# Kernel optimization log

Hardware: AMD Instinct MI355X
Metric: run time of the kernel (lower is better)

Reference implementation:

```python
import jax, jax.numpy as jnp
import numpy as np

N_NODES = 100000
N_EDGES = 3200000
IN_DIM = 128


def setup_inputs() -> dict:
    key = jax.random.key(0)
    ks = jax.random.split(key, 6)
    x = jax.random.normal(ks[0], (N_NODES, IN_DIM), dtype=jnp.float32)
    edge_index = jax.random.randint(ks[1], (2, N_EDGES), 0, N_NODES, dtype=jnp.int64)
    # Glorot-ish init for weights, zero bias (PyG GCNConv default has bias)
    W1 = jax.random.normal(ks[2], (IN_DIM, 32), dtype=jnp.float32) / np.sqrt(IN_DIM)
    b1 = jnp.zeros((32,), dtype=jnp.float32)
    W2 = jax.random.normal(ks[3], (32, 16), dtype=jnp.float32) / np.sqrt(32.0)
    b2 = jnp.zeros((16,), dtype=jnp.float32)
    Wf = jax.random.normal(ks[4], (16, 1), dtype=jnp.float32) / np.sqrt(16.0)
    bf = jnp.zeros((1,), dtype=jnp.float32)
    return {"x": x, "edge_index": edge_index, "W1": W1, "b1": b1,
            "W2": W2, "b2": b2, "Wf": Wf, "bf": bf}


def reference(x, edge_index, W1, b1, W2, b2, Wf, bf):
    N = x.shape[0]
    # PyG GCNConv: add self-loops, symmetric normalization D^-1/2 (A+I) D^-1/2
    loop = jnp.arange(N, dtype=edge_index.dtype)
    src = jnp.concatenate([edge_index[0], loop])  # message sources (x_j)
    dst = jnp.concatenate([edge_index[1], loop])  # aggregation targets
    deg = jax.ops.segment_sum(jnp.ones_like(dst, dtype=x.dtype), dst, num_segments=N)
    dinv = jax.lax.rsqrt(jnp.maximum(deg, 1.0))  # deg >= 1 due to self-loops
    norm = dinv[src] * dinv[dst]                  # per-edge coefficient

    def gcn_conv(h, W, b):
        h = h @ W                                 # linear transform first (small dim)
        msg = h[src] * norm[:, None]              # gather + scale
        return jax.ops.segment_sum(msg, dst, num_segments=N) + b  # scatter-add

    h = jax.nn.relu(gcn_conv(x, W1, b1))
    h = jax.nn.relu(gcn_conv(h, W2, b2))
    return (h @ Wf + bf).squeeze(-1)              # [N]
```

## Files before the change

kernel.cpp:

```cpp
#include <hip/hip_runtime.h>


#define TPB 256
#define NBUCK 256
#define BCAP 16384
#define CHUNK 8192

__device__ __forceinline__ unsigned f2bf(float f) {
    unsigned u = __float_as_uint(f);
    return (u + 0x7FFFu + ((u >> 16) & 1u)) >> 16;
}
__device__ __forceinline__ float bflo(unsigned u) { return __uint_as_float(u << 16); }
__device__ __forceinline__ float bfhi(unsigned u) { return __uint_as_float(u & 0xFFFF0000u); }

__global__ void zero_bcursor_kernel(int* __restrict__ bcur) {
    bcur[threadIdx.x] = 0;
}

__global__ __launch_bounds__(256) void binA2_kernel(
        const int* __restrict__ src, const int* __restrict__ dst,
        int* __restrict__ bcur, unsigned* __restrict__ staging, int E, int NPB) {
    __shared__ unsigned packed[CHUNK];
    __shared__ unsigned char buckb[CHUNK];
    __shared__ int hist[NBUCK];
    __shared__ int scan_[NBUCK];
    __shared__ int lstart[NBUCK];
    __shared__ int lcur[NBUCK];
    __shared__ int gbase[NBUCK];
    int tid = threadIdx.x;
    int start = blockIdx.x * CHUNK;
    int sz = min(CHUNK, E - start);

    hist[tid] = 0;
    __syncthreads();
    for (int i = tid; i < sz; i += 256) {
        unsigned d = (unsigned)dst[start + i];
        atomicAdd(&hist[d / (unsigned)NPB], 1);
    }
    __syncthreads();
    int v = hist[tid];
    scan_[tid] = v;
    __syncthreads();
    for (int dd = 1; dd < NBUCK; dd <<= 1) {
        int t = 0;
        if (tid >= dd) t = scan_[tid - dd];
        __syncthreads();
        scan_[tid] += t;
        __syncthreads();
    }
    lstart[tid] = scan_[tid] - v;
    lcur[tid] = 0;
    gbase[tid] = atomicAdd(&bcur[tid], v);
    __syncthreads();
    for (int i = tid; i < sz; i += 256) {
        unsigned d = (unsigned)dst[start + i];
        unsigned s = (unsigned)src[start + i];
        unsigned b = d / (unsigned)NPB;
        unsigned loc = d - b * (unsigned)NPB;
        int pos = atomicAdd(&lcur[b], 1);
        int si = lstart[b] + pos;
        packed[si] = (loc << 20) | s;
        buckb[si] = (unsigned char)b;
    }
    __syncthreads();
    for (int i = tid; i < sz; i += 256) {
        unsigned b = buckb[i];
        int dsti = gbase[b] + (i - lstart[b]);
        if (dsti < BCAP)
            staging[(size_t)b * BCAP + dsti] = packed[i];
    }
}

__global__ void bucket_scan_kernel(const int* __restrict__ bcur, int* __restrict__ bbase) {
    __shared__ int s[NBUCK];
    int tid = threadIdx.x;
    int v = min(bcur[tid], BCAP);
    s[tid] = v;
    __syncthreads();
    for (int d = 1; d < NBUCK; d <<= 1) {
        int t = 0;
        if (tid >= d) t = s[tid - d];
        __syncthreads();
        s[tid] += t;
        __syncthreads();
    }
    bbase[tid] = s[tid] - v;
}

__global__ void buildB_kernel(const int* __restrict__ bcur, const int* __restrict__ bbase,
                              const unsigned* __restrict__ staging,
                              int* __restrict__ offs, int* __restrict__ counts,
                              float* __restrict__ dinv, int* __restrict__ csr_src,
                              int N, int NPB) {
    __shared__ int hist[512];
    __shared__ int scan_[512];
    __shared__ int cur[512];
    int b = blockIdx.x;
    int tid = threadIdx.x;
    int sz = min(bcur[b], BCAP);
    int base = bbase[b];
    int n0 = b * NPB;
    int nn = min(NPB, N - n0);
    const unsigned* se = staging + (size_t)b * BCAP;

    hist[tid] = 0;
    __syncthreads();
    for (int i = tid; i < sz; i += 512)
        atomicAdd(&hist[se[i] >> 20], 1);
    __syncthreads();
    int h = hist[tid];
    scan_[tid] = h;
    __syncthreads();
    for (int d = 1; d < 512; d <<= 1) {
        int t = 0;
        if (tid >= d) t = scan_[tid - d];
        __syncthreads();
        scan_[tid] += t;
        __syncthreads();
    }
    int excl = scan_[tid] - h;
    cur[tid] = excl;
    if (tid < nn) {
        int node = n0 + tid;
        offs[node] = base + excl;
        counts[node] = h;
        dinv[node] = rsqrtf((float)(h + 1));
    }
    __syncthreads();
    for (int i = tid; i < sz; i += 512) {
        unsigned p = se[i];
        int pos = atomicAdd(&cur[p >> 20], 1);
        csr_src[base + pos] = (int)(p & 0xFFFFFu);
    }
}

__global__ __launch_bounds__(256) void gemm1_kernel(
        const float* __restrict__ x, const float* __restrict__ W1,
        const float* __restrict__ dinv, unsigned* __restrict__ xwd, int N) {
    __shared__ float ws_[128 * 32];
    for (int i = threadIdx.x; i < 128 * 32; i += blockDim.x) ws_[i] = W1[i];
    __syncthreads();
    int t = threadIdx.x;
    int node = blockIdx.x * 64 + (t >> 2);
    if (node >= N) return;
    int jq = (t & 3) * 8;
    float acc[8];
#pragma unroll
    for (int j = 0; j < 8; ++j) acc[j] = 0.0f;
    const float4* xr = (const float4*)(x + (size_t)node * 128);
#pragma unroll 4
    for (int k4 = 0; k4 < 32; ++k4) {
        float4 xv = xr[k4];
        const float* wb = ws_ + (k4 * 4) * 32 + jq;
        float4 a0 = *(const float4*)(wb);
        float4 a1 = *(const float4*)(wb + 4);
        float4 b0 = *(const float4*)(wb + 32);
        float4 b1v = *(const float4*)(wb + 36);
        float4 c0 = *(const float4*)(wb + 64);
        float4 c1 = *(const float4*)(wb + 68);
        float4 d0 = *(const float4*)(wb + 96);
        float4 d1 = *(const float4*)(wb + 100);
        acc[0] += xv.x * a0.x + xv.y * b0.x + xv.z * c0.x + xv.w * d0.x;
        acc[1] += xv.x * a0.y + xv.y * b0.y + xv.z * c0.y + xv.w * d0.y;
        acc[2] += xv.x * a0.z + xv.y * b0.z + xv.z * c0.z + xv.w * d0.z;
        acc[3] += xv.x * a0.w + xv.y * b0.w + xv.z * c0.w + xv.w * d0.w;
        acc[4] += xv.x * a1.x + xv.y * b1v.x + xv.z * c1.x + xv.w * d1.x;
        acc[5] += xv.x * a1.y + xv.y * b1v.y + xv.z * c1.y + xv.w * d1.y;
        acc[6] += xv.x * a1.z + xv.y * b1v.z + xv.z * c1.z + xv.w * d1.z;
        acc[7] += xv.x * a1.w + xv.y * b1v.w + xv.z * c1.w + xv.w * d1.w;
    }
    float d = dinv[node];
    unsigned pk0 = f2bf(acc[0] * d) | (f2bf(acc[1] * d) << 16);
    unsigned pk1 = f2bf(acc[2] * d) | (f2bf(acc[3] * d) << 16);
    unsigned pk2 = f2bf(acc[4] * d) | (f2bf(acc[5] * d) << 16);
    unsigned pk3 = f2bf(acc[6] * d) | (f2bf(acc[7] * d) << 16);
    ((uint4*)(xwd + (size_t)node * 16))[t & 3] = make_uint4(pk0, pk1, pk2, pk3);
}

__global__ void agg32h_kernel(const int* __restrict__ offs, const int* __restrict__ counts,
                              const int* __restrict__ csr_src, const float* __restrict__ dinv,
                              const unsigned* __restrict__ xwd, float* __restrict__ agg, int N) {
    int wave = threadIdx.x >> 6;
    int lane = threadIdx.x & 63;
    int node = blockIdx.x * 4 + wave;
    if (node >= N) return;
    int q = lane & 3;
    int g = lane >> 2;
    int off = offs[node];
    int deg = counts[node];
    float acc[8];
#pragma unroll
    for (int k = 0; k < 8; ++k) acc[k] = 0.f;
    if (g == 0) {
        uint4 v = ((const uint4*)(xwd + (size_t)node * 16))[q];
        acc[0] = bflo(v.x); acc[1] = bfhi(v.x);
        acc[2] = bflo(v.y); acc[3] = bfhi(v.y);
        acc[4] = bflo(v.z); acc[5] = bfhi(v.z);
        acc[6] = bflo(v.w); acc[7] = bfhi(v.w);
    }
    int i = g;
    for (; i + 16 < deg; i += 32) {
        int s0 = csr_src[off + i];
        int s1 = csr_src[off + i + 16];
        uint4 v0 = ((const uint4*)(xwd + (size_t)s0 * 16))[q];
        uint4 v1 = ((const uint4*)(xwd + (size_t)s1 * 16))[q];
        acc[0] += bflo(v0.x) + bflo(v1.x); acc[1] += bfhi(v0.x) + bfhi(v1.x);
        acc[2] += bflo(v0.y) + bflo(v1.y); acc[3] += bfhi(v0.y) + bfhi(v1.y);
        acc[4] += bflo(v0.z) + bflo(v1.z); acc[5] += bfhi(v0.z) + bfhi(v1.z);
        acc[6] += bflo(v0.w) + bflo(v1.w); acc[7] += bfhi(v0.w) + bfhi(v1.w);
    }
    for (; i < deg; i += 16) {
        int s = csr_src[off + i];
        uint4 v = ((const uint4*)(xwd + (size_t)s * 16))[q];
        acc[0] += bflo(v.x); acc[1] += bfhi(v.x);
        acc[2] += bflo(v.y); acc[3] += bfhi(v.y);
        acc[4] += bflo(v.z); acc[5] += bfhi(v.z);
        acc[6] += bflo(v.w); acc[7] += bfhi(v.w);
    }
#pragma unroll
    for (int d = 32; d >= 4; d >>= 1) {
#pragma unroll
        for (int k = 0; k < 8; ++k) acc[k] += __shfl_down(acc[k], d, 64);
    }
    if (g == 0) {
        float dv = dinv[node];
        float* op = agg + (size_t)node * 32 + q * 8;
        ((float4*)op)[0] = make_float4(acc[0] * dv, acc[1] * dv, acc[2] * dv, acc[3] * dv);
        ((float4*)op)[1] = make_float4(acc[4] * dv, acc[5] * dv, acc[6] * dv, acc[7] * dv);
    }
}

__global__ void gemm2_kernel(const float* __restrict__ agg1, const float* __restrict__ W2,
                             const float* __restrict__ b1, const float* __restrict__ dinv,
                             unsigned* __restrict__ h2wd, int N) {
    __shared__ float ws_[32 * 16];
    __shared__ float bs_[32];
    for (int i = threadIdx.x; i < 32 * 16; i += blockDim.x) ws_[i] = W2[i];
    if (threadIdx.x < 32) bs_[threadIdx.x] = b1[threadIdx.x];
    __syncthreads();
    int node = blockIdx.x * blockDim.x + threadIdx.x;
    if (node >= N) return;
    float h[32];
    const float4* ar = (const float4*)(agg1 + (size_t)node * 32);
#pragma unroll
    for (int k4 = 0; k4 < 8; ++k4) {
        float4 v = ar[k4];
        h[k4 * 4 + 0] = fmaxf(v.x + bs_[k4 * 4 + 0], 0.0f);
        h[k4 * 4 + 1] = fmaxf(v.y + bs_[k4 * 4 + 1], 0.0f);
        h[k4 * 4 + 2] = fmaxf(v.z + bs_[k4 * 4 + 2], 0.0f);
        h[k4 * 4 + 3] = fmaxf(v.w + bs_[k4 * 4 + 3], 0.0f);
    }
    float acc[16];
#pragma unroll
    for (int j = 0; j < 16; ++j) acc[j] = 0.0f;
#pragma unroll
    for (int k = 0; k < 32; ++k) {
        float hv = h[k];
#pragma unroll
        for (int j4 = 0; j4 < 4; ++j4) {
            float4 w = *(const float4*)(ws_ + k * 16 + j4 * 4);
            acc[j4 * 4 + 0] += hv * w.x;
            acc[j4 * 4 + 1] += hv * w.y;
            acc[j4 * 4 + 2] += hv * w.z;
            acc[j4 * 4 + 3] += hv * w.w;
        }
    }
    float d = dinv[node];
    unsigned pk[8];
#pragma unroll
    for (int j = 0; j < 8; ++j)
        pk[j] = f2bf(acc[2 * j] * d) | (f2bf(acc[2 * j + 1] * d) << 16);
    uint4* hp = (uint4*)(h2wd + (size_t)node * 8);
    hp[0] = make_uint4(pk[0], pk[1], pk[2], pk[3]);
    hp[1] = make_uint4(pk[4], pk[5], pk[6], pk[7]);
}

__global__ void agg16h_kernel(const int* __restrict__ offs, const int* __restrict__ counts,
                              const int* __restrict__ csr_src, const float* __restrict__ dinv,
                              const unsigned* __restrict__ h2wd, float* __restrict__ agg, int N) {
    int wave = threadIdx.x >> 6;
    int lane = threadIdx.x & 63;
    int node = blockIdx.x * 4 + wave;
    if (node >= N) return;
    int q = lane & 1;
    int g = lane >> 1;
    int off = offs[node];
    int deg = counts[node];
    float acc[8];
#pragma unroll
    for (int k = 0; k < 8; ++k) acc[k] = 0.f;
    if (g == 0) {
        uint4 v = ((const uint4*)(h2wd + (size_t)node * 8))[q];
        acc[0] = bflo(v.x); acc[1] = bfhi(v.x);
        acc[2] = bflo(v.y); acc[3] = bfhi(v.y);
        acc[4] = bflo(v.z); acc[5] = bfhi(v.z);
        acc[6] = bflo(v.w); acc[7] = bfhi(v.w);
    }
    for (int i = g; i < deg; i += 32) {
        int s = csr_src[off + i];
        uint4 v = ((const uint4*)(h2wd + (size_t)s * 8))[q];
        acc[0] += bflo(v.x); acc[1] += bfhi(v.x);
        acc[2] += bflo(v.y); acc[3] += bfhi(v.y);
        acc[4] += bflo(v.z); acc[5] += bfhi(v.z);
        acc[6] += bflo(v.w); acc[7] += bfhi(v.w);
    }
#pragma unroll
    for (int d = 32; d >= 2; d >>= 1) {
#pragma unroll
        for (int k = 0; k < 8; ++k) acc[k] += __shfl_down(acc[k], d, 64);
    }
    if (g == 0) {
        float dv = dinv[node];
        float* op = agg + (size_t)node * 16 + q * 8;
        ((float4*)op)[0] = make_float4(acc[0] * dv, acc[1] * dv, acc[2] * dv, acc[3] * dv);
        ((float4*)op)[1] = make_float4(acc[4] * dv, acc[5] * dv, acc[6] * dv, acc[7] * dv);
    }
}

__global__ void final_kernel(const float* __restrict__ agg2, const float* __restrict__ b2,
                             const float* __restrict__ Wf, const float* __restrict__ bf,
                             float* __restrict__ out, int N) {
    int i = blockIdx.x * blockDim.x + threadIdx.x;
    if (i >= N) return;
    const float4* ar = (const float4*)(agg2 + (size_t)i * 16);
    float acc = bf[0];
#pragma unroll
    for (int j4 = 0; j4 < 4; ++j4) {
        float4 v = ar[j4];
        acc += fmaxf(v.x + b2[j4 * 4 + 0], 0.0f) * Wf[j4 * 4 + 0];
        acc += fmaxf(v.y + b2[j4 * 4 + 1], 0.0f) * Wf[j4 * 4 + 1];
        acc += fmaxf(v.z + b2[j4 * 4 + 2], 0.0f) * Wf[j4 * 4 + 2];
        acc += fmaxf(v.w + b2[j4 * 4 + 3], 0.0f) * Wf[j4 * 4 + 3];
    }
    out[i] = acc;
}

extern "C" void kernel_launch(void* const* d_in, const int* in_sizes, int n_in,
                              void* d_out, int out_size, void* d_ws, size_t ws_size,
                              hipStream_t stream) {
    const float* x  = (const float*)d_in[0];
    const int*   ei = (const int*)d_in[1];
    const float* W1 = (const float*)d_in[2];
    const float* b1 = (const float*)d_in[3];
    const float* W2 = (const float*)d_in[4];
    const float* b2 = (const float*)d_in[5];
    const float* Wf = (const float*)d_in[6];
    const float* bf = (const float*)d_in[7];

    int N = in_sizes[0] / 128;
    int E = in_sizes[1] / 2;
    const int* src = ei;
    const int* dst = ei + E;
    int NPB = (N + NBUCK - 1) / NBUCK;

    size_t Np = ((size_t)N + 3) & ~(size_t)3;
    size_t Ep = ((size_t)E + 3) & ~(size_t)3;
    int* wsI      = (int*)d_ws;
    int* counts   = wsI;
    int* offs     = counts + Np;
    int* bcur     = offs + Np;
    int* bbase    = bcur + NBUCK;
    int* csr_src  = bbase + NBUCK;
    float* dinv   = (float*)(csr_src + Ep);
    unsigned* xwd = (unsigned*)(dinv + Np);
    float* agg1   = (float*)(xwd + 16 * Np);
    unsigned* h2wd= (unsigned*)(agg1 + 32 * Np);
    float* agg2   = (float*)(h2wd + 8 * Np);
    float* out    = (float*)d_out;
    unsigned* staging = (unsigned*)agg1;

    int nbG1 = (N + 63) / 64;
    int nbC = (E + CHUNK - 1) / CHUNK;
    int nbN = (N + TPB - 1) / TPB;
    int nbW = (N + 3) / 4;

    zero_bcursor_kernel<<<1, NBUCK, 0, stream>>>(bcur);
    binA2_kernel<<<nbC, 256, 0, stream>>>(src, dst, bcur, staging, E, NPB);
    bucket_scan_kernel<<<1, NBUCK, 0, stream>>>(bcur, bbase);
    buildB_kernel<<<NBUCK, 512, 0, stream>>>(bcur, bbase, staging, offs, counts,
                                             dinv, csr_src, N, NPB);
    gemm1_kernel<<<nbG1, 256, 0, stream>>>(x, W1, dinv, xwd, N);
    agg32h_kernel<<<nbW, TPB, 0, stream>>>(offs, counts, csr_src, dinv, xwd, agg1, N);
    gemm2_kernel<<<nbN, TPB, 0, stream>>>(agg1, W2, b1, dinv, h2wd, N);
    agg16h_kernel<<<nbW, TPB, 0, stream>>>(offs, counts, csr_src, dinv, h2wd, agg2, N);
    final_kernel<<<nbN, TPB, 0, stream>>>(agg2, b2, Wf, bf, out, N);
}
```

Before: 286.5 us.

## Remap aggregation to few lanes per node and fuse final layer

Both aggregation kernels now give each node 4 lanes (layer 1) or 2 lanes (layer 2) instead of a full 64-lane wave. Each lane walks the whole neighbor list serially with 2-way unrolling, so the cross-lane shuffle reductions go away. With an average degree near 33, the old mapping left many lanes idle; the new one raises occupancy per node but serializes the neighbor walk and makes the CSR index reads less coalesced. The final linear+ReLU layer is fused into the second aggregation, which removes the agg2 round trip and one launch.

Result: no change. 284.9 us (-0.6%).

```diff
diff --git a/kernel.cpp b/kernel.cpp
--- a/kernel.cpp
+++ b/kernel.cpp
@@ -177,31 +177,28 @@
     ((uint4*)(xwd + (size_t)node * 16))[t & 3] = make_uint4(pk0, pk1, pk2, pk3);
 }
 
-__global__ void agg32h_kernel(const int* __restrict__ offs, const int* __restrict__ counts,
-                              const int* __restrict__ csr_src, const float* __restrict__ dinv,
-                              const unsigned* __restrict__ xwd, float* __restrict__ agg, int N) {
-    int wave = threadIdx.x >> 6;
-    int lane = threadIdx.x & 63;
-    int node = blockIdx.x * 4 + wave;
+__global__ __launch_bounds__(256) void aggS32_kernel(
+        const int* __restrict__ offs, const int* __restrict__ counts,
+        const int* __restrict__ csr_src, const float* __restrict__ dinv,
+        const unsigned* __restrict__ xwd, float* __restrict__ agg, int N) {
+    int t = threadIdx.x;
+    int q = t & 3;
+    int node = blockIdx.x * 64 + (t >> 2);
     if (node >= N) return;
-    int q = lane & 3;
-    int g = lane >> 2;
     int off = offs[node];
     int deg = counts[node];
     float acc[8];
-#pragma unroll
-    for (int k = 0; k < 8; ++k) acc[k] = 0.f;
-    if (g == 0) {
+    {
         uint4 v = ((const uint4*)(xwd + (size_t)node * 16))[q];
         acc[0] = bflo(v.x); acc[1] = bfhi(v.x);
         acc[2] = bflo(v.y); acc[3] = bfhi(v.y);
         acc[4] = bflo(v.z); acc[5] = bfhi(v.z);
         acc[6] = bflo(v.w); acc[7] = bfhi(v.w);
     }
-    int i = g;
-    for (; i + 16 < deg; i += 32) {
+    int i = 0;
+    for (; i + 1 < deg; i += 2) {
         int s0 = csr_src[off + i];
-        int s1 = csr_src[off + i + 16];
+        int s1 = csr_src[off + i + 1];
         uint4 v0 = ((const uint4*)(xwd + (size_t)s0 * 16))[q];
         uint4 v1 = ((const uint4*)(xwd + (size_t)s1 * 16))[q];
         acc[0] += bflo(v0.x) + bflo(v1.x); acc[1] += bfhi(v0.x) + bfhi(v1.x);
@@ -209,7 +206,7 @@
         acc[4] += bflo(v0.z) + bflo(v1.z); acc[5] += bfhi(v0.z) + bfhi(v1.z);
         acc[6] += bflo(v0.w) + bflo(v1.w); acc[7] += bfhi(v0.w) + bfhi(v1.w);
     }
-    for (; i < deg; i += 16) {
+    if (i < deg) {
         int s = csr_src[off + i];
         uint4 v = ((const uint4*)(xwd + (size_t)s * 16))[q];
         acc[0] += bflo(v.x); acc[1] += bfhi(v.x);
@@ -217,17 +214,10 @@
         acc[4] += bflo(v.z); acc[5] += bfhi(v.z);
         acc[6] += bflo(v.w); acc[7] += bfhi(v.w);
     }
-#pragma unroll
-    for (int d = 32; d >= 4; d >>= 1) {
-#pragma unroll
-        for (int k = 0; k < 8; ++k) acc[k] += __shfl_down(acc[k], d, 64);
-    }
-    if (g == 0) {
-        float dv = dinv[node];
-        float* op = agg + (size_t)node * 32 + q * 8;
-        ((float4*)op)[0] = make_float4(acc[0] * dv, acc[1] * dv, acc[2] * dv, acc[3] * dv);
-        ((float4*)op)[1] = make_float4(acc[4] * dv, acc[5] * dv, acc[6] * dv, acc[7] * dv);
-    }
+    float dv = dinv[node];
+    float* op = agg + (size_t)node * 32 + q * 8;
+    ((float4*)op)[0] = make_float4(acc[0] * dv, acc[1] * dv, acc[2] * dv, acc[3] * dv);
+    ((float4*)op)[1] = make_float4(acc[4] * dv, acc[5] * dv, acc[6] * dv, acc[7] * dv);
 }
 
 __global__ void gemm2_kernel(const float* __restrict__ agg1, const float* __restrict__ W2,
@@ -275,28 +265,44 @@
     hp[1] = make_uint4(pk[4], pk[5], pk[6], pk[7]);
 }
 
-__global__ void agg16h_kernel(const int* __restrict__ offs, const int* __restrict__ counts,
-                              const int* __restrict__ csr_src, const float* __restrict__ dinv,
-                              const unsigned* __restrict__ h2wd, float* __restrict__ agg, int N) {
-    int wave = threadIdx.x >> 6;
-    int lane = threadIdx.x & 63;
-    int node = blockIdx.x * 4 + wave;
+__global__ __launch_bounds__(256) void aggS16f_kernel(
+        const int* __restrict__ offs, const int* __restrict__ counts,
+        const int* __restrict__ csr_src, const float* __restrict__ dinv,
+        const unsigned* __restrict__ h2wd,
+        const float* __restrict__ b2, const float* __restrict__ Wf,
+        const float* __restrict__ bf, float* __restrict__ out, int N) {
+    __shared__ float bs_[16];
+    __shared__ float wf_[16];
+    __shared__ float bfv;
+    int t = threadIdx.x;
+    if (t < 16) { bs_[t] = b2[t]; wf_[t] = Wf[t]; }
+    if (t == 0) bfv = bf[0];
+    __syncthreads();
+    int q = t & 1;
+    int node = blockIdx.x * 128 + (t >> 1);
     if (node >= N) return;
-    int q = lane & 1;
-    int g = lane >> 1;
     int off = offs[node];
     int deg = counts[node];
     float acc[8];
-#pragma unroll
-    for (int k = 0; k < 8; ++k) acc[k] = 0.f;
-    if (g == 0) {
+    {
         uint4 v = ((const uint4*)(h2wd + (size_t)node * 8))[q];
         acc[0] = bflo(v.x); acc[1] = bfhi(v.x);
         acc[2] = bflo(v.y); acc[3] = bfhi(v.y);
         acc[4] = bflo(v.z); acc[5] = bfhi(v.z);
         acc[6] = bflo(v.w); acc[7] = bfhi(v.w);
     }
-    for (int i = g; i < deg; i += 32) {
+    int i = 0;
+    for (; i + 1 < deg; i += 2) {
+        int s0 = csr_src[off + i];
+        int s1 = csr_src[off + i + 1];
+        uint4 v0 = ((const uint4*)(h2wd + (size_t)s0 * 8))[q];
+        uint4 v1 = ((const uint4*)(h2wd + (size_t)s1 * 8))[q];
+        acc[0] += bflo(v0.x) + bflo(v1.x); acc[1] += bfhi(v0.x) + bfhi(v1.x);
+        acc[2] += bflo(v0.y) + bflo(v1.y); acc[3] += bfhi(v0.y) + bfhi(v1.y);
+        acc[4] += bflo(v0.z) + bflo(v1.z); acc[5] += bfhi(v0.z) + bfhi(v1.z);
+        acc[6] += bflo(v0.w) + bflo(v1.w); acc[7] += bfhi(v0.w) + bfhi(v1.w);
+    }
+    if (i < deg) {
         int s = csr_src[off + i];
         uint4 v = ((const uint4*)(h2wd + (size_t)s * 8))[q];
         acc[0] += bflo(v.x); acc[1] += bfhi(v.x);
@@ -304,35 +310,15 @@
         acc[4] += bflo(v.z); acc[5] += bfhi(v.z);
         acc[6] += bflo(v.w); acc[7] += bfhi(v.w);
     }
-#pragma unroll
-    for (int d = 32; d >= 2; d >>= 1) {
-#pragma unroll
-        for (int k = 0; k < 8; ++k) acc[k] += __shfl_down(acc[k], d, 64);
-    }
-    if (g == 0) {
-        float dv = dinv[node];
-        float* op = agg + (size_t)node * 16 + q * 8;
-        ((float4*)op)[0] = make_float4(acc[0] * dv, acc[1] * dv, acc[2] * dv, acc[3] * dv);
-        ((float4*)op)[1] = make_float4(acc[4] * dv, acc[5] * dv, acc[6] * dv, acc[7] * dv);
-    }
-}
-
-__global__ void final_kernel(const float* __restrict__ agg2, const float* __restrict__ b2,
-                             const float* __restrict__ Wf, const float* __restrict__ bf,
-                             float* __restrict__ out, int N) {
-    int i = blockIdx.x * blockDim.x + threadIdx.x;
-    if (i >= N) return;
-    const float4* ar = (const float4*)(agg2 + (size_t)i * 16);
-    float acc = bf[0];
-#pragma unroll
-    for (int j4 = 0; j4 < 4; ++j4) {
-        float4 v = ar[j4];
-        acc += fmaxf(v.x + b2[j4 * 4 + 0], 0.0f) * Wf[j4 * 4 + 0];
-        acc += fmaxf(v.y + b2[j4 * 4 + 1], 0.0f) * Wf[j4 * 4 + 1];
-        acc += fmaxf(v.z + b2[j4 * 4 + 2], 0.0f) * Wf[j4 * 4 + 2];
-        acc += fmaxf(v.w + b2[j4 * 4 + 3], 0.0f) * Wf[j4 * 4 + 3];
-    }
-    out[i] = acc;
+    float dv = dinv[node];
+    const float* bq = bs_ + q * 8;
+    const float* wq = wf_ + q * 8;
+    float part = 0.f;
+#pragma unroll
+    for (int k = 0; k < 8; ++k)
+        part += fmaxf(acc[k] * dv + bq[k], 0.f) * wq[k];
+    part += __shfl_xor(part, 1, 64);
+    if (q == 0) out[node] = part + bfv;
 }
 
 extern "C" void kernel_launch(void* const* d_in, const int* in_sizes, int n_in,
@@ -365,14 +351,14 @@
     unsigned* xwd = (unsigned*)(dinv + Np);
     float* agg1   = (float*)(xwd + 16 * Np);
     unsigned* h2wd= (unsigned*)(agg1 + 32 * Np);
-    float* agg2   = (float*)(h2wd + 8 * Np);
     float* out    = (float*)d_out;
     unsigned* staging = (unsigned*)agg1;
 
     int nbG1 = (N + 63) / 64;
-    int nbC = (E + CHUNK - 1) / CHUNK;
-    int nbN = (N + TPB - 1) / TPB;
-    int nbW = (N + 3) / 4;
+    int nbC  = (E + CHUNK - 1) / CHUNK;
+    int nbN  = (N + TPB - 1) / TPB;
+    int nbA32 = (N + 63) / 64;
+    int nbA16 = (N + 127) / 128;
 
     zero_bcursor_kernel<<<1, NBUCK, 0, stream>>>(bcur);
     binA2_kernel<<<nbC, 256, 0, stream>>>(src, dst, bcur, staging, E, NPB);
@@ -380,8 +366,8 @@
     buildB_kernel<<<NBUCK, 512, 0, stream>>>(bcur, bbase, staging, offs, counts,
                                              dinv, csr_src, N, NPB);
     gemm1_kernel<<<nbG1, 256, 0, stream>>>(x, W1, dinv, xwd, N);
-    agg32h_kernel<<<nbW, TPB, 0, stream>>>(offs, counts, csr_src, dinv, xwd, agg1, N);
+    aggS32_kernel<<<nbA32, 256, 0, stream>>>(offs, counts, csr_src, dinv, xwd, agg1, N);
     gemm2_kernel<<<nbN, TPB, 0, stream>>>(agg1, W2, b1, dinv, h2wd, N);
-    agg16h_kernel<<<nbW, TPB, 0, stream>>>(offs, counts, csr_src, dinv, h2wd, agg2, N);
-    final_kernel<<<nbN, TPB, 0, stream>>>(agg2, b2, Wf, bf, out, N);
-}
+    aggS16f_kernel<<<nbA16, 256, 0, stream>>>(offs, counts, csr_src, dinv, h2wd,
+                                              b2, Wf, bf, out, N);
+}
```
